# Performance work log

Measured on AMD Instinct MI355X. Metric: run time of the kernel, lower is better.

Reference implementation:

```python
import jax, jax.numpy as jnp
import numpy as np

E = 32  # gate matrix size (hard-coded in module)


def build_gates():
    g = np.array([1.0 - 2.0 ** (-i / 32.0 * 5.0 - 1.0) for i in range(E)], dtype=np.float32)
    G = np.diag(g).astype(np.float32)
    for i in range(1, E):
        G[i, i - 1] = 1.0 - g[i]
    return jnp.asarray(G)


def mat_scan(state, g):
    # Inclusive matrix-gated prefix scan along axis 1.
    # state: [B, L, D, E], g: [B, L, E, E]
    # out[t] = sum_{j<=t} state[j] @ (g[j+1] @ ... @ g[t])
    def combine(a, b):
        sa, ga = a
        sb, gb = b
        return (jnp.matmul(sa, gb) + sb, jnp.matmul(ga, gb))
    out, _ = jax.lax.associative_scan(combine, (state, g), axis=1)
    return out


def setup_inputs() -> dict:
    key = jax.random.key(0)
    ks = jax.random.split(key, 8)
    B, L, D = 1, 1024, 1024
    nheads, kvheads, dk, dv = 32, 32, 32, 32
    std = 0.02
    q = jax.random.normal(ks[0], (B, L, D), dtype=jnp.float32)
    k = jax.random.normal(ks[1], (B, L, D), dtype=jnp.float32)
    v = jax.random.normal(ks[2], (B, L, D), dtype=jnp.float32)
    Wq = jax.random.normal(ks[3], (nheads * dk, D), dtype=jnp.float32) * std
    Wk = jax.random.normal(ks[4], (kvheads * dk, D), dtype=jnp.float32) * std
    Wv = jax.random.normal(ks[5], (kvheads * dv, D), dtype=jnp.float32) * std
    Wd = jax.random.normal(ks[6], (D, nheads * dv), dtype=jnp.float32) * std
    gates = build_gates()
    return {"q": q, "k": k, "v": v, "Wq": Wq, "Wk": Wk, "Wv": Wv, "Wd": Wd, "gates": gates}


def reference(q, k, v, Wq, Wk, Wv, Wd, gates):
    B, Lq, _ = q.shape
    Lk = k.shape[1]
    nheads, kvheads, dk, dv = 32, 32, 32, 32
    scale = dk ** 0.25
    queries = (q @ Wq.T).reshape(B, Lq, nheads, dk) / scale
    keys = (k @ Wk.T) / scale                      # [B, Lk, kvh*dk]
    values = v @ Wv.T                              # [B, Lk, kvh*dv]
    g = jnp.broadcast_to(gates[None, None], (B, Lk, E, E))
    # pad to scan width E=32 (keys) / kvheads=32 (values), as in the module
    keys_s = jnp.pad(keys[..., None], ((0, 0), (0, 0), (0, 0), (0, E - 1)))
    keys_s = mat_scan(keys_s, g).reshape(B, Lk, kvheads, dk, E)
    vals_s = jnp.pad(values[..., None], ((0, 0), (0, 0), (0, 0), (0, kvheads - 1)))
    vals_s = mat_scan(vals_s, g).reshape(B, Lk, kvheads, dv, E)
    # expansion = nheads // kvheads == 1, no head replication needed
    qk = jnp.einsum('blhd,blhde->blhe', queries, keys_s)
    attn = jax.nn.softmax(qk, axis=3)
    qkv = jnp.einsum('blhe,blhde->blhd', attn, vals_s)
    z = qkv.reshape(B, Lq, nheads * dv)
    return z @ Wd.T
```

## Files before the change

### kernel.cpp

```cpp
#include <hip/hip_runtime.h>

#define D_DIM 1024
#define L_DIM 1024

typedef _Float16 half8 __attribute__((ext_vector_type(8)));
typedef float f32x4 __attribute__((ext_vector_type(4)));

__device__ __forceinline__ ushort4 cvt4f(const float4& x) {
    ushort4 h;
    h.x = __builtin_bit_cast(unsigned short, (_Float16)x.x);
    h.y = __builtin_bit_cast(unsigned short, (_Float16)x.y);
    h.z = __builtin_bit_cast(unsigned short, (_Float16)x.z);
    h.w = __builtin_bit_cast(unsigned short, (_Float16)x.w);
    return h;
}
__device__ __forceinline__ float4 h4tof4(const ushort4& u) {
    float4 r;
    r.x = (float)__builtin_bit_cast(_Float16, u.x);
    r.y = (float)__builtin_bit_cast(_Float16, u.y);
    r.z = (float)__builtin_bit_cast(_Float16, u.z);
    r.w = (float)__builtin_bit_cast(_Float16, u.w);
    return r;
}

__device__ __forceinline__ void async16(const void* g, void* l) {
    __builtin_amdgcn_global_load_lds(
        (const __attribute__((address_space(1))) void*)g,
        (__attribute__((address_space(3))) void*)l, 16, 0, 0);
}

#define ETB 16

__global__ __launch_bounds__(256) void prep_kernel(
    const float* __restrict__ q, const float* __restrict__ k,
    const float* __restrict__ v, const float* __restrict__ Wq,
    const float* __restrict__ Wk, const float* __restrict__ Wv,
    const float* __restrict__ Wd, const float* __restrict__ gates,
    ushort* qf, ushort* wq, ushort* wk, ushort* wv, ushort* wd,
    ushort* kf, ushort* vf) {
    const int tid = threadIdx.x;
    const int z = blockIdx.y;
    if (z <= 4) {
        const float* src = (z == 0) ? q : (z == 1) ? Wq : (z == 2) ? Wk
                          : (z == 3) ? Wv : Wd;
        ushort* dst = (z == 0) ? qf : (z == 1) ? wq : (z == 2) ? wk
                     : (z == 3) ? wv : wd;
        for (int i = blockIdx.x * 256 + tid; i < 262144; i += 16384) {
            ((ushort4*)dst)[i] = cvt4f(((const float4*)src)[i]);
        }
    } else {
        const float* src = (z == 5) ? k : v;
        ushort* dst = (z == 5) ? kf : vf;
        const int c = tid << 2;
        const int t0 = blockIdx.x * ETB;
        const float g = gates[0];
        float4 a = make_float4(0.f, 0.f, 0.f, 0.f);
        int s0 = t0 - 32;
        if (s0 < 0) s0 = 0;
        for (int s = s0; s < t0 + ETB; ++s) {
            const float4 x = *(const float4*)(src + (size_t)s * D_DIM + c);
            a.x = fmaf(g, a.x, x.x);
            a.y = fmaf(g, a.y, x.y);
            a.z = fmaf(g, a.z, x.z);
            a.w = fmaf(g, a.w, x.w);
            if (s >= t0) {
                ((ushort4*)dst)[(size_t)s * (D_DIM / 4) + (c >> 2)] = cvt4f(a);
            }
        }
    }
}

template <typename OutT>
__device__ __forceinline__ void gemm1_core(const ushort* __restrict__ A,
                                           const ushort* __restrict__ B,
                                           OutT* __restrict__ C, int kbeg,
                                           int kend) {
    __shared__ ushort sA[2][8192];
    __shared__ ushort sB[2][4096];

    const int tid = threadIdx.x;
    const int bx = blockIdx.x, by = blockIdx.y;
    const int w = tid >> 6, l = tid & 63;
    const int wm = w >> 1, wn = w & 1;
    const int lr = l & 15, lg = l >> 4;

    const int tb = tid * 16;
    int aLds[2];
    size_t aG[2];
#pragma unroll
    for (int i = 0; i < 2; ++i) {
        const int off = i * 8192 + tb;
        const int row = off >> 7, colb = off & 127;
        aLds[i] = off;
        aG[i] = (size_t)(by * 128 + row) * 2048 + (colb ^ ((row & 7) << 4));
    }
    int aLds4[4];
    size_t aG4[4];
#pragma unroll
    for (int i = 0; i < 4; ++i) {
        const int off = i * 4096 + tb;
        const int row = off >> 7, colb = off & 127;
        aLds4[i] = off;
        aG4[i] = (size_t)(by * 128 + row) * 2048 + (colb ^ ((row & 7) << 4));
    }
    int bLds[2];
    size_t bG[2];
#pragma unroll
    for (int i = 0; i < 2; ++i) {
        const int off = i * 4096 + tb;
        const int row = off >> 7, colb = off & 127;
        bLds[i] = off;
        bG[i] = (size_t)(bx * 64 + row) * 2048 + (colb ^ ((row & 7) << 4));
    }
    int aBase[4], aMask[4];
#pragma unroll
    for (int i = 0; i < 4; ++i) {
        const int row = wm * 64 + i * 16 + lr;
        aBase[i] = row * 128;
        aMask[i] = (row & 7) << 4;
    }
    int bBase[2], bMask[2];
#pragma unroll
    for (int j = 0; j < 2; ++j) {
        const int row = wn * 32 + j * 16 + lr;
        bBase[j] = row * 128;
        bMask[j] = (row & 7) << 4;
    }

    f32x4 acc[4][2] = {};
    const char* A_c = (const char*)A;
    const char* B_c = (const char*)B;

#define STAGE(buf, k0)                                                       \
    {                                                                        \
        const size_t kb = (size_t)(k0) * 2;                                  \
        _Pragma("unroll") for (int i = 0; i < 4; ++i) {                      \
            async16(A_c + aG4[i] + kb, (char*)&sA[buf][0] + aLds4[i]);       \
        }                                                                    \
        _Pragma("unroll") for (int i = 0; i < 2; ++i) {                      \
            async16(B_c + bG[i] + kb, (char*)&sB[buf][0] + bLds[i]);         \
        }                                                                    \
    }

    const int nt = (kend - kbeg) >> 6;
    STAGE(0, kbeg);
    __syncthreads();

    for (int t = 0; t < nt; ++t) {
        const int cur = t & 1;
        if (t + 1 < nt) STAGE(cur ^ 1, kbeg + (t + 1) * 64);
#pragma unroll
        for (int ks = 0; ks < 2; ++ks) {
            const int colb = ks * 64 + lg * 16;
            half8 af[4], bf[2];
#pragma unroll
            for (int i = 0; i < 4; ++i) {
                af[i] = *(const half8*)((const char*)&sA[cur][0] +
                                        (aBase[i] + (colb ^ aMask[i])));
            }
#pragma unroll
            for (int j = 0; j < 2; ++j) {
                bf[j] = *(const half8*)((const char*)&sB[cur][0] +
                                        (bBase[j] + (colb ^ bMask[j])));
            }
#pragma unroll
            for (int i = 0; i < 4; ++i)
#pragma unroll
                for (int j = 0; j < 2; ++j) {
                    acc[i][j] = __builtin_amdgcn_mfma_f32_16x16x32_f16(
                        af[i], bf[j], acc[i][j], 0, 0, 0);
                }
        }
        __syncthreads();
    }
#undef STAGE

#pragma unroll
    for (int i = 0; i < 4; ++i)
#pragma unroll
        for (int j = 0; j < 2; ++j) {
            const size_t r0 = (size_t)(by * 128 + wm * 64 + i * 16 + lg * 4);
            const int col = bx * 64 + wn * 32 + j * 16 + lr;
            if constexpr (sizeof(OutT) == 2) {
                ushort* Cp = (ushort*)C + r0 * D_DIM + col;
#pragma unroll
                for (int rr = 0; rr < 4; ++rr)
                    Cp[(size_t)rr * D_DIM] = __builtin_bit_cast(
                        unsigned short, (_Float16)acc[i][j][rr]);
            } else {
                float* Cp = (float*)C + r0 * D_DIM + col;
#pragma unroll
                for (int rr = 0; rr < 4; ++rr)
                    Cp[(size_t)rr * D_DIM] = acc[i][j][rr];
            }
        }
}

__global__ __launch_bounds__(256, 3) void qkv_gemm_kernel(
    const ushort* qf, const ushort* kf, const ushort* vf, const ushort* wq,
    const ushort* wk, const ushort* wv, ushort* Qm, ushort* Km, ushort* Vm) {
    const ushort *A, *B;
    ushort* C;
    if (blockIdx.z == 0)      { A = qf; B = wq; C = Qm; }
    else if (blockIdx.z == 1) { A = kf; B = wk; C = Km; }
    else                      { A = vf; B = wv; C = Vm; }
    gemm1_core<ushort>(A, B, C, 0, 1024);
}

__global__ __launch_bounds__(256, 3) void out_gemm_kernel(
    const ushort* zf, const ushort* wd, float* P0, float* P1) {
    float* C = blockIdx.z ? P1 : P0;
    const int kb = blockIdx.z * 512;
    gemm1_core<float>(zf, wd, C, kb, kb + 512);
}

#define GTB 4

__global__ __launch_bounds__(256) void gate_kernel(
    const ushort* __restrict__ Qm, const ushort* __restrict__ Km,
    const ushort* __restrict__ Vm, ushort* __restrict__ zf) {
    const int tid = threadIdx.x;
    const int c4 = tid;
    const float invs = 0.17677669529663687f;
#pragma unroll
    for (int r = 0; r < GTB; ++r) {
        const int t = blockIdx.x * GTB + r;
        const size_t o = (size_t)t * 256 + c4;
        const float4 qv = h4tof4(((const ushort4*)Qm)[o]);
        const float4 kv = h4tof4(((const ushort4*)Km)[o]);
        const float4 vv = h4tof4(((const ushort4*)Vm)[o]);
        float p = qv.x * kv.x + qv.y * kv.y + qv.z * kv.z + qv.w * kv.w;
        p += __shfl_xor(p, 1);
        p += __shfl_xor(p, 2);
        p += __shfl_xor(p, 4);
        const float a = 1.0f / (1.0f + 31.0f * __expf(-p * invs));
        float4 z;
        z.x = a * vv.x;
        z.y = a * vv.y;
        z.z = a * vv.z;
        z.w = a * vv.w;
        ((ushort4*)zf)[o] = cvt4f(z);
    }
}

__global__ __launch_bounds__(256) void add_kernel(const float* __restrict__ P0,
                                                  const float* __restrict__ P1,
                                                  float* __restrict__ out) {
#pragma unroll
    for (int u = 0; u < 4; ++u) {
        const int i = blockIdx.x * 1024 + u * 256 + threadIdx.x;
        float4 a = ((const float4*)P0)[i];
        float4 b = ((const float4*)P1)[i];
        float4 o;
        o.x = a.x + b.x;
        o.y = a.y + b.y;
        o.z = a.z + b.z;
        o.w = a.w + b.w;
        ((float4*)out)[i] = o;
    }
}

extern "C" void kernel_launch(void* const* d_in, const int* in_sizes, int n_in,
                              void* d_out, int out_size, void* d_ws,
                              size_t ws_size, hipStream_t stream) {
    const float* q     = (const float*)d_in[0];
    const float* k     = (const float*)d_in[1];
    const float* v     = (const float*)d_in[2];
    const float* Wq    = (const float*)d_in[3];
    const float* Wk    = (const float*)d_in[4];
    const float* Wv    = (const float*)d_in[5];
    const float* Wd    = (const float*)d_in[6];
    const float* gates = (const float*)d_in[7];
    float* out = (float*)d_out;

    char* ws = (char*)d_ws;
    const size_t MB = 1024 * 1024;
    ushort* qf = (ushort*)(ws + 0 * MB);
    ushort* wq = (ushort*)(ws + 2 * MB);
    ushort* wk = (ushort*)(ws + 4 * MB);
    ushort* wv = (ushort*)(ws + 6 * MB);
    ushort* wd = (ushort*)(ws + 8 * MB);
    ushort* kf = (ushort*)(ws + 10 * MB);
    ushort* vf = (ushort*)(ws + 12 * MB);
    ushort* Qm = (ushort*)(ws + 14 * MB);
    ushort* Km = (ushort*)(ws + 16 * MB);
    ushort* Vm = (ushort*)(ws + 18 * MB);
    ushort* zf = (ushort*)(ws + 20 * MB);
    float* P0  = (float*)(ws + 22 * MB);
    float* P1  = (float*)(ws + 26 * MB);

    prep_kernel<<<dim3(64, 7), 256, 0, stream>>>(q, k, v, Wq, Wk, Wv, Wd,
                                                 gates, qf, wq, wk, wv, wd,
                                                 kf, vf);
    qkv_gemm_kernel<<<dim3(16, 8, 3), 256, 0, stream>>>(qf, kf, vf, wq, wk,
                                                        wv, Qm, Km, Vm);
    gate_kernel<<<dim3(L_DIM / GTB), 256, 0, stream>>>(Qm, Km, Vm, zf);
    out_gemm_kernel<<<dim3(16, 8, 2), 256, 0, stream>>>(zf, wd, P0, P1);
    add_kernel<<<dim3(256), 256, 0, stream>>>(P0, P1, out);
}
```

Measured before the change: 126.9 us.

## Fuse QKV GEMMs with gating epilogue and drop split-K output GEMM

```diff
diff --git a/kernel.cpp b/kernel.cpp
--- a/kernel.cpp
+++ b/kernel.cpp
@@ -13,14 +13,6 @@
     h.z = __builtin_bit_cast(unsigned short, (_Float16)x.z);
     h.w = __builtin_bit_cast(unsigned short, (_Float16)x.w);
     return h;
-}
-__device__ __forceinline__ float4 h4tof4(const ushort4& u) {
-    float4 r;
-    r.x = (float)__builtin_bit_cast(_Float16, u.x);
-    r.y = (float)__builtin_bit_cast(_Float16, u.y);
-    r.z = (float)__builtin_bit_cast(_Float16, u.z);
-    r.w = (float)__builtin_bit_cast(_Float16, u.w);
-    return r;
 }
 
 __device__ __forceinline__ void async16(const void* g, void* l) {
@@ -70,13 +62,13 @@
     }
 }
 
-template <typename OutT>
-__device__ __forceinline__ void gemm1_core(const ushort* __restrict__ A,
-                                           const ushort* __restrict__ B,
-                                           OutT* __restrict__ C, int kbeg,
-                                           int kend) {
-    __shared__ ushort sA[2][8192];
-    __shared__ ushort sB[2][4096];
+__global__ __launch_bounds__(256, 1) void qkvz_kernel(
+    const ushort* __restrict__ qf, const ushort* __restrict__ kf,
+    const ushort* __restrict__ vf, const ushort* __restrict__ wq,
+    const ushort* __restrict__ wk, const ushort* __restrict__ wv,
+    ushort* __restrict__ zf) {
+    __shared__ ushort sA[2][3][4096];
+    __shared__ ushort sB[2][3][4096];
 
     const int tid = threadIdx.x;
     const int bx = blockIdx.x, by = blockIdx.y;
@@ -85,86 +77,170 @@
     const int lr = l & 15, lg = l >> 4;
 
     const int tb = tid * 16;
-    int aLds[2];
-    size_t aG[2];
-#pragma unroll
-    for (int i = 0; i < 2; ++i) {
-        const int off = i * 8192 + tb;
-        const int row = off >> 7, colb = off & 127;
-        aLds[i] = off;
-        aG[i] = (size_t)(by * 128 + row) * 2048 + (colb ^ ((row & 7) << 4));
-    }
-    int aLds4[4];
-    size_t aG4[4];
-#pragma unroll
-    for (int i = 0; i < 4; ++i) {
+    int ldsOff[2];
+    size_t gA[2], gB[2];
+#pragma unroll
+    for (int i = 0; i < 2; ++i) {
         const int off = i * 4096 + tb;
         const int row = off >> 7, colb = off & 127;
-        aLds4[i] = off;
-        aG4[i] = (size_t)(by * 128 + row) * 2048 + (colb ^ ((row & 7) << 4));
-    }
-    int bLds[2];
-    size_t bG[2];
+        ldsOff[i] = off;
+        gA[i] = (size_t)(by * 64 + row) * 2048 + (colb ^ ((row & 7) << 4));
+        gB[i] = (size_t)(bx * 64 + row) * 2048 + (colb ^ ((row & 7) << 4));
+    }
+    int aBase[2], aMask[2], bBase[2], bMask[2];
+#pragma unroll
+    for (int i = 0; i < 2; ++i) {
+        const int rowA = wm * 32 + i * 16 + lr;
+        aBase[i] = rowA * 128;
+        aMask[i] = (rowA & 7) << 4;
+        const int rowB = wn * 32 + i * 16 + lr;
+        bBase[i] = rowB * 128;
+        bMask[i] = (rowB & 7) << 4;
+    }
+
+    f32x4 acc[3][2][2] = {};
+    const char* Ap[3] = {(const char*)qf, (const char*)kf, (const char*)vf};
+    const char* Bp[3] = {(const char*)wq, (const char*)wk, (const char*)wv};
+
+#define STAGE3(buf, k0)                                                       \
+    {                                                                         \
+        const size_t kb = (size_t)(k0) * 2;                                   \
+        _Pragma("unroll") for (int m = 0; m < 3; ++m) {                       \
+            _Pragma("unroll") for (int i = 0; i < 2; ++i) {                   \
+                async16(Ap[m] + gA[i] + kb, (char*)&sA[buf][m][0] + ldsOff[i]); \
+                async16(Bp[m] + gB[i] + kb, (char*)&sB[buf][m][0] + ldsOff[i]); \
+            }                                                                 \
+        }                                                                     \
+    }
+
+    STAGE3(0, 0);
+    __syncthreads();
+
+    for (int t = 0; t < 16; ++t) {
+        const int cur = t & 1;
+        if (t < 15) STAGE3(cur ^ 1, (t + 1) * 64);
+#pragma unroll
+        for (int ks = 0; ks < 2; ++ks) {
+            const int colb = ks * 64 + lg * 16;
+            half8 af[3][2], bf[3][2];
+#pragma unroll
+            for (int m = 0; m < 3; ++m)
+#pragma unroll
+                for (int i = 0; i < 2; ++i) {
+                    af[m][i] = *(const half8*)((const char*)&sA[cur][m][0] +
+                                               (aBase[i] + (colb ^ aMask[i])));
+                    bf[m][i] = *(const half8*)((const char*)&sB[cur][m][0] +
+                                               (bBase[i] + (colb ^ bMask[i])));
+                }
+#pragma unroll
+            for (int m = 0; m < 3; ++m)
+#pragma unroll
+                for (int i = 0; i < 2; ++i)
+#pragma unroll
+                    for (int j = 0; j < 2; ++j) {
+                        acc[m][i][j] = __builtin_amdgcn_mfma_f32_16x16x32_f16(
+                            af[m][i], bf[m][j], acc[m][i][j], 0, 0, 0);
+                    }
+        }
+        __syncthreads();
+    }
+#undef STAGE3
+
+    const float invs = 0.17677669529663687f;
+#pragma unroll
+    for (int i = 0; i < 2; ++i) {
+        f32x4 p;
+#pragma unroll
+        for (int r = 0; r < 4; ++r)
+            p[r] = acc[0][i][0][r] * acc[1][i][0][r] +
+                   acc[0][i][1][r] * acc[1][i][1][r];
+#pragma unroll
+        for (int m = 1; m <= 8; m <<= 1) {
+#pragma unroll
+            for (int r = 0; r < 4; ++r) p[r] += __shfl_xor(p[r], m);
+        }
+        f32x4 a;
+#pragma unroll
+        for (int r = 0; r < 4; ++r)
+            a[r] = 1.0f / (1.0f + 31.0f * __expf(-p[r] * invs));
+#pragma unroll
+        for (int j = 0; j < 2; ++j) {
+            const size_t r0 = (size_t)(by * 64 + wm * 32 + i * 16 + lg * 4);
+            ushort* Zp = zf + r0 * D_DIM + bx * 64 + wn * 32 + j * 16 + lr;
+#pragma unroll
+            for (int r = 0; r < 4; ++r)
+                Zp[(size_t)r * D_DIM] = __builtin_bit_cast(
+                    unsigned short, (_Float16)(a[r] * acc[2][i][j][r]));
+        }
+    }
+}
+
+__global__ __launch_bounds__(256) void out_gemm_kernel(
+    const ushort* __restrict__ zin, const ushort* __restrict__ wd,
+    float* __restrict__ out) {
+    __shared__ ushort sA[2][4096];
+    __shared__ ushort sB[2][4096];
+
+    const int tid = threadIdx.x;
+    const int bx = blockIdx.x, by = blockIdx.y;
+    const int w = tid >> 6, l = tid & 63;
+    const int wm = w >> 1, wn = w & 1;
+    const int lr = l & 15, lg = l >> 4;
+
+    const int tb = tid * 16;
+    int ldsOff[2];
+    size_t gA[2], gB[2];
 #pragma unroll
     for (int i = 0; i < 2; ++i) {
         const int off = i * 4096 + tb;
         const int row = off >> 7, colb = off & 127;
-        bLds[i] = off;
-        bG[i] = (size_t)(bx * 64 + row) * 2048 + (colb ^ ((row & 7) << 4));
-    }
-    int aBase[4], aMask[4];
-#pragma unroll
-    for (int i = 0; i < 4; ++i) {
-        const int row = wm * 64 + i * 16 + lr;
-        aBase[i] = row * 128;
-        aMask[i] = (row & 7) << 4;
-    }
-    int bBase[2], bMask[2];
-#pragma unroll
-    for (int j = 0; j < 2; ++j) {
-        const int row = wn * 32 + j * 16 + lr;
-        bBase[j] = row * 128;
-        bMask[j] = (row & 7) << 4;
-    }
-
-    f32x4 acc[4][2] = {};
-    const char* A_c = (const char*)A;
-    const char* B_c = (const char*)B;
-
-#define STAGE(buf, k0)                                                       \
+        ldsOff[i] = off;
+        gA[i] = (size_t)(by * 64 + row) * 2048 + (colb ^ ((row & 7) << 4));
+        gB[i] = (size_t)(bx * 64 + row) * 2048 + (colb ^ ((row & 7) << 4));
+    }
+    int aBase[2], aMask[2], bBase[2], bMask[2];
+#pragma unroll
+    for (int i = 0; i < 2; ++i) {
+        const int rowA = wm * 32 + i * 16 + lr;
+        aBase[i] = rowA * 128;
+        aMask[i] = (rowA & 7) << 4;
+        const int rowB = wn * 32 + i * 16 + lr;
+        bBase[i] = rowB * 128;
+        bMask[i] = (rowB & 7) << 4;
+    }
+
+    f32x4 acc[2][2] = {};
+    const char* A_c = (const char*)zin;
+    const char* B_c = (const char*)wd;
+
+#define STAGE1(buf, k0)                                                      \
     {                                                                        \
         const size_t kb = (size_t)(k0) * 2;                                  \
-        _Pragma("unroll") for (int i = 0; i < 4; ++i) {                      \
-            async16(A_c + aG4[i] + kb, (char*)&sA[buf][0] + aLds4[i]);       \
+        _Pragma("unroll") for (int i = 0; i < 2; ++i) {                      \
+            async16(A_c + gA[i] + kb, (char*)&sA[buf][0] + ldsOff[i]);       \
+            async16(B_c + gB[i] + kb, (char*)&sB[buf][0] + ldsOff[i]);       \
         }                                                                    \
-        _Pragma("unroll") for (int i = 0; i < 2; ++i) {                      \
-            async16(B_c + bG[i] + kb, (char*)&sB[buf][0] + bLds[i]);         \
-        }                                                                    \
-    }
-
-    const int nt = (kend - kbeg) >> 6;
-    STAGE(0, kbeg);
+    }
+
+    STAGE1(0, 0);
     __syncthreads();
 
-    for (int t = 0; t < nt; ++t) {
+    for (int t = 0; t < 16; ++t) {
         const int cur = t & 1;
-        if (t + 1 < nt) STAGE(cur ^ 1, kbeg + (t + 1) * 64);
+        if (t < 15) STAGE1(cur ^ 1, (t + 1) * 64);
 #pragma unroll
         for (int ks = 0; ks < 2; ++ks) {
             const int colb = ks * 64 + lg * 16;
-            half8 af[4], bf[2];
-#pragma unroll
-            for (int i = 0; i < 4; ++i) {
+            half8 af[2], bf[2];
+#pragma unroll
+            for (int i = 0; i < 2; ++i) {
                 af[i] = *(const half8*)((const char*)&sA[cur][0] +
                                         (aBase[i] + (colb ^ aMask[i])));
+                bf[i] = *(const half8*)((const char*)&sB[cur][0] +
+                                        (bBase[i] + (colb ^ bMask[i])));
             }
 #pragma unroll
-            for (int j = 0; j < 2; ++j) {
-                bf[j] = *(const half8*)((const char*)&sB[cur][0] +
-                                        (bBase[j] + (colb ^ bMask[j])));
-            }
-#pragma unroll
-            for (int i = 0; i < 4; ++i)
+            for (int i = 0; i < 2; ++i)
 #pragma unroll
                 for (int j = 0; j < 2; ++j) {
                     acc[i][j] = __builtin_amdgcn_mfma_f32_16x16x32_f16(
@@ -173,91 +249,17 @@
         }
         __syncthreads();
     }
-#undef STAGE
-
-#pragma unroll
-    for (int i = 0; i < 4; ++i)
+#undef STAGE1
+
+#pragma unroll
+    for (int i = 0; i < 2; ++i)
 #pragma unroll
         for (int j = 0; j < 2; ++j) {
-            const size_t r0 = (size_t)(by * 128 + wm * 64 + i * 16 + lg * 4);
-            const int col = bx * 64 + wn * 32 + j * 16 + lr;
-            if constexpr (sizeof(OutT) == 2) {
-                ushort* Cp = (ushort*)C + r0 * D_DIM + col;
-#pragma unroll
-                for (int rr = 0; rr < 4; ++rr)
-                    Cp[(size_t)rr * D_DIM] = __builtin_bit_cast(
-                        unsigned short, (_Float16)acc[i][j][rr]);
-            } else {
-                float* Cp = (float*)C + r0 * D_DIM + col;
-#pragma unroll
-                for (int rr = 0; rr < 4; ++rr)
-                    Cp[(size_t)rr * D_DIM] = acc[i][j][rr];
-            }
-        }
-}
-
-__global__ __launch_bounds__(256, 3) void qkv_gemm_kernel(
-    const ushort* qf, const ushort* kf, const ushort* vf, const ushort* wq,
-    const ushort* wk, const ushort* wv, ushort* Qm, ushort* Km, ushort* Vm) {
-    const ushort *A, *B;
-    ushort* C;
-    if (blockIdx.z == 0)      { A = qf; B = wq; C = Qm; }
-    else if (blockIdx.z == 1) { A = kf; B = wk; C = Km; }
-    else                      { A = vf; B = wv; C = Vm; }
-    gemm1_core<ushort>(A, B, C, 0, 1024);
-}
-
-__global__ __launch_bounds__(256, 3) void out_gemm_kernel(
-    const ushort* zf, const ushort* wd, float* P0, float* P1) {
-    float* C = blockIdx.z ? P1 : P0;
-    const int kb = blockIdx.z * 512;
-    gemm1_core<float>(zf, wd, C, kb, kb + 512);
-}
-
-#define GTB 4
-
-__global__ __launch_bounds__(256) void gate_kernel(
-    const ushort* __restrict__ Qm, const ushort* __restrict__ Km,
-    const ushort* __restrict__ Vm, ushort* __restrict__ zf) {
-    const int tid = threadIdx.x;
-    const int c4 = tid;
-    const float invs = 0.17677669529663687f;
-#pragma unroll
-    for (int r = 0; r < GTB; ++r) {
-        const int t = blockIdx.x * GTB + r;
-        const size_t o = (size_t)t * 256 + c4;
-        const float4 qv = h4tof4(((const ushort4*)Qm)[o]);
-        const float4 kv = h4tof4(((const ushort4*)Km)[o]);
-        const float4 vv = h4tof4(((const ushort4*)Vm)[o]);
-        float p = qv.x * kv.x + qv.y * kv.y + qv.z * kv.z + qv.w * kv.w;
-        p += __shfl_xor(p, 1);
-        p += __shfl_xor(p, 2);
-        p += __shfl_xor(p, 4);
-        const float a = 1.0f / (1.0f + 31.0f * __expf(-p * invs));
-        float4 z;
-        z.x = a * vv.x;
-        z.y = a * vv.y;
-        z.z = a * vv.z;
-        z.w = a * vv.w;
-        ((ushort4*)zf)[o] = cvt4f(z);
-    }
-}
-
-__global__ __launch_bounds__(256) void add_kernel(const float* __restrict__ P0,
-                                                  const float* __restrict__ P1,
-                                                  float* __restrict__ out) {
-#pragma unroll
-    for (int u = 0; u < 4; ++u) {
-        const int i = blockIdx.x * 1024 + u * 256 + threadIdx.x;
-        float4 a = ((const float4*)P0)[i];
-        float4 b = ((const float4*)P1)[i];
-        float4 o;
-        o.x = a.x + b.x;
-        o.y = a.y + b.y;
-        o.z = a.z + b.z;
-        o.w = a.w + b.w;
-        ((float4*)out)[i] = o;
-    }
+            float* Cp = out + (size_t)(by * 64 + wm * 32 + i * 16 + lg * 4) * D_DIM
+                            + bx * 64 + wn * 32 + j * 16 + lr;
+#pragma unroll
+            for (int r = 0; r < 4; ++r) Cp[(size_t)r * D_DIM] = acc[i][j][r];
+        }
 }
 
 extern "C" void kernel_launch(void* const* d_in, const int* in_sizes, int n_in,
@@ -282,19 +284,11 @@
     ushort* wd = (ushort*)(ws + 8 * MB);
     ushort* kf = (ushort*)(ws + 10 * MB);
     ushort* vf = (ushort*)(ws + 12 * MB);
-    ushort* Qm = (ushort*)(ws + 14 * MB);
-    ushort* Km = (ushort*)(ws + 16 * MB);
-    ushort* Vm = (ushort*)(ws + 18 * MB);
-    ushort* zf = (ushort*)(ws + 20 * MB);
-    float* P0  = (float*)(ws + 22 * MB);
-    float* P1  = (float*)(ws + 26 * MB);
+    ushort* zf = (ushort*)(ws + 14 * MB);
 
     prep_kernel<<<dim3(64, 7), 256, 0, stream>>>(q, k, v, Wq, Wk, Wv, Wd,
                                                  gates, qf, wq, wk, wv, wd,
                                                  kf, vf);
-    qkv_gemm_kernel<<<dim3(16, 8, 3), 256, 0, stream>>>(qf, kf, vf, wq, wk,
-                                                        wv, Qm, Km, Vm);
-    gate_kernel<<<dim3(L_DIM / GTB), 256, 0, stream>>>(Qm, Km, Vm, zf);
-    out_gemm_kernel<<<dim3(16, 8, 2), 256, 0, stream>>>(zf, wd, P0, P1);
-    add_kernel<<<dim3(256), 256, 0, stream>>>(P0, P1, out);
-}
+    qkvz_kernel<<<dim3(16, 16), 256, 0, stream>>>(qf, kf, vf, wq, wk, wv, zf);
+    out_gemm_kernel<<<dim3(16, 16), 256, 0, stream>>>(zf, wd, out);
+}
```

Result: slower. 130.8 us (+3.1%).
